# Optimization experiments

Hardware: AMD Instinct MI355X
Metric: run time of the kernel (lower is better)

## Reference

```python
import jax, jax.numpy as jnp
import numpy as np

RADIUS = 0.1
WEIGHT = 0.2
MATMUL_NORM = False


def setup_inputs() -> dict:
    key = jax.random.key(0)
    k1, k2, k3, k4, k5 = jax.random.split(key, 5)
    S, B, Ck, Cv, H, W = 8, 2, 64, 64, 64, 64
    return {
        "memory_keys": jax.random.normal(k1, (S, B, Ck, H, W), jnp.float32),
        "memory_values": jax.random.normal(k2, (S, B, Cv, H, W), jnp.float32),
        "query_query": jax.random.normal(k3, (B, Ck, H, W), jnp.float32),
        "disparity": jax.random.normal(k4, (B, 1, H, W), jnp.float32),
        "sequence_index": jax.random.randint(k5, (B, S, 2), 0, 10, jnp.int32),
    }


def reference(memory_keys, memory_values, query_query, disparity, sequence_index):
    S, B, Ck, H, W = memory_keys.shape
    Cv = memory_values.shape[2]
    HW, SHW = H * W, S * H * W

    # keys: [B, Ck, S*H*W]; queries: [B, H*W, Ck]
    keys = jnp.transpose(memory_keys, (1, 2, 0, 3, 4)).reshape(B, Ck, SHW)
    q = jnp.transpose(query_query.reshape(B, Ck, HW), (0, 2, 1))

    # disparity-based additive mask, vectorized over frames
    weight = WEIGHT / S / H / W
    idx = sequence_index.astype(jnp.float32)
    dist = jnp.sqrt((idx[:, :, 1] - 5.0) ** 2 + (idx[:, :, 0] - 5.0) ** 2)  # [B, S]
    total_disp = dist[:, :, None, None] * disparity  # [B, S, H, W] (disparity [B,1,H,W])
    mask = jnp.where(jnp.abs(total_disp) > RADIUS, weight, 0.0).reshape(B, 1, SHW)

    attn = jnp.einsum("bnc,bcm->bnm", q, keys)  # [B, HW, SHW]
    if MATMUL_NORM:
        attn = attn * (Ck ** -0.5)
    attn = jax.nn.softmax(attn, axis=-1) + mask

    vals = jnp.transpose(memory_values, (1, 0, 3, 4, 2)).reshape(B, SHW, Cv)
    out = jnp.einsum("bnm,bmv->bnv", attn, vals)  # [B, HW, Cv]
    return jnp.transpose(out, (0, 2, 1)).reshape(B, Cv, H, W)
```

## Files before the change

### kernel.cpp

```cpp
#include <hip/hip_runtime.h>
#include <hip/hip_bf16.h>
#include <stdint.h>

#define NS   8
#define NB   2
#define CK   64
#define CV   64
#define HWN  4096
#define SHW  32768
#define RADIUS_ 0.1f
#define MASK_W  6.103515625e-6f

#define TM    32
#define NW    8
#define QS_STR 68
#define P_STR  40
#define SBIAS 24.0f
#define LOG2E 1.4426950408889634f
#define SBIAS2 34.624680981135326f
#define KS    4

#define KT_ELEMS (NS * NB * CK * HWN)
#define KT_BYTES ((size_t)KT_ELEMS * 2)
#define VB_BYTES ((size_t)KT_ELEMS * 2)
#define MASK_OFF (KT_BYTES + VB_BYTES)
#define WS_NEED  (MASK_OFF + (size_t)NB * CV * 4)
#define ONUM_OFF (MASK_OFF + 4096)
#define ONUM_BYTES ((size_t)KS * NB * HWN * CV * 4)
#define ODEN_OFF (ONUM_OFF + ONUM_BYTES)
#define ODEN_BYTES ((size_t)KS * NB * HWN * 4)
#define WS2      (ODEN_OFF + ODEN_BYTES)

typedef __bf16    bf16x8 __attribute__((ext_vector_type(8)));
typedef _Float16  f16x8  __attribute__((ext_vector_type(8)));
typedef float     f32x4  __attribute__((ext_vector_type(4)));
typedef unsigned short u16x8 __attribute__((ext_vector_type(8)));
typedef uint32_t  u32x2 __attribute__((ext_vector_type(2)));
typedef uint32_t  u32x4 __attribute__((ext_vector_type(4)));

__device__ __forceinline__ unsigned short f2bfu(float x) {
  __hip_bfloat16 h = __float2bfloat16(x);
  return __builtin_bit_cast(unsigned short, h);
}
__device__ __forceinline__ bf16x8 ld_bf8_lds(const unsigned short* p) {
  u16x8 u = *(const u16x8*)p;
  return __builtin_bit_cast(bf16x8, u);
}
__device__ __forceinline__ void load_lds16(const void* g, void* l) {
  __builtin_amdgcn_global_load_lds(
      (const __attribute__((address_space(1))) unsigned int*)g,
      (__attribute__((address_space(3))) unsigned int*)l, 16, 0, 0);
}

#define PK_STR 72
__global__ __launch_bounds__(512) void prep_all(
    const float* __restrict__ keys, const float* __restrict__ vals,
    const float* __restrict__ disp, const int* __restrict__ seq,
    _Float16* __restrict__ kT, unsigned short* __restrict__ vbf,
    float* __restrict__ maskadd)
{
  const int t = threadIdx.x;
  const int blk = blockIdx.x;
  if (blk < 256) {
    __shared__ _Float16 lds[256 * PK_STR];
    const int chunk = blk & 15;
    const int s     = (blk >> 4) & 7;
    const int b     = blk >> 7;
    const int hw0   = chunk * 256;
    const int c_st  = t >> 3;
    const int msub  = (t & 7) * 8;

    const float* krow = keys + ((size_t)((s * NB + b) * CK + c_st)) * HWN + hw0;
    #pragma unroll
    for (int r = 0; r < 4; ++r) {
      const int m0 = msub + r * 64;
      f32x4 k0 = *(const f32x4*)(krow + m0);
      f32x4 k1 = *(const f32x4*)(krow + m0 + 4);
      #pragma unroll
      for (int j = 0; j < 4; ++j) {
        lds[(m0 + j)     * PK_STR + c_st] = (_Float16)k0[j];
        lds[(m0 + 4 + j) * PK_STR + c_st] = (_Float16)k1[j];
      }
    }
    __syncthreads();

    _Float16* kout = kT + ((size_t)(b * SHW + s * HWN + hw0)) * CK;
    const int mm = t >> 3, c0 = (t & 7) * 8;
    #pragma unroll
    for (int r2 = 0; r2 < 4; ++r2) {
      const int m = mm + r2 * 64;
      u16x8 v = *(const u16x8*)&lds[m * PK_STR + c0];
      *(u16x8*)(kout + (size_t)m * CK + c0) = v;
    }
  } else {
    const int r = blk - 256;
    const int s = r >> 7;
    const int b = (r >> 6) & 1;
    const int c = r & 63;
    float j0 = (float)seq[(b * NS + s) * 2 + 0];
    float j1 = (float)seq[(b * NS + s) * 2 + 1];
    const float dist = sqrtf((j1 - 5.f) * (j1 - 5.f) + (j0 - 5.f) * (j0 - 5.f));

    const size_t i = (size_t)r * HWN + t * 8;
    const int hw = t * 8;
    f32x4 a  = *(const f32x4*)(vals + i);
    f32x4 bb = *(const f32x4*)(vals + i + 4);
    f32x4 d0 = *(const f32x4*)(disp + (size_t)b * HWN + hw);
    f32x4 d1 = *(const f32x4*)(disp + (size_t)b * HWN + hw + 4);
    u16x8 o;
    float acc = 0.f;
    #pragma unroll
    for (int j = 0; j < 4; ++j) {
      o[j]     = f2bfu(a[j]);
      o[4 + j] = f2bfu(bb[j]);
      if (fabsf(dist * d0[j]) > RADIUS_) acc += a[j];
      if (fabsf(dist * d1[j]) > RADIUS_) acc += bb[j];
    }
    *(u16x8*)(vbf + i) = o;

    #pragma unroll
    for (int m = 32; m >= 1; m >>= 1) acc += __shfl_xor(acc, m);
    __shared__ float red[8];
    if ((t & 63) == 0) red[t >> 6] = acc;
    __syncthreads();
    if (t == 0) {
      float s8 = 0.f;
      #pragma unroll
      for (int j = 0; j < 8; ++j) s8 += red[j];
      atomicAdd(&maskadd[b * CV + c], MASK_W * s8);
    }
  }
}

struct __align__(16) Smem6 {
  union {
    struct {
      _Float16       kbuf[2][128 * 64];
      unsigned short vbuf[2][64 * 128];
    } main;
    struct {
      float obuf[4][32][64];
      float dbuf[4][32];
    } epi;
    float qs[64 * QS_STR];
  };
};

__global__ __launch_bounds__(512, 4) void attn_v6(
    const _Float16* __restrict__ kT,
    const unsigned short* __restrict__ vbf,
    const float* __restrict__ query,
    float* __restrict__ onum,
    float* __restrict__ odenom)
{
  __shared__ Smem6 sm;
  const int t    = threadIdx.x;
  const int w    = t >> 6;
  const int lane = t & 63;
  const int quad = lane >> 4;
  const int l15  = lane & 15;
  const int kq   = w & 3;
  const int rg   = w >> 2;
  const int bidx = blockIdx.x;
  const int xcd  = bidx & 7;
  const int b    = xcd & 1;
  const int ks   = xcd >> 1;
  const int tile = bidx >> 3;
  const int n0   = tile * 64;

  {
    const int qc   = t >> 3;
    const int noff = (t & 7) * 8;
    const int slot = qc ^ ((t & 7) << 2);
    const float* qp = query + (size_t)(b * CK + qc) * HWN + n0 + noff;
    f32x4 q0 = *(const f32x4*)(qp);
    f32x4 q1 = *(const f32x4*)(qp + 4);
    #pragma unroll
    for (int j = 0; j < 4; ++j) {
      sm.qs[(noff + j)     * QS_STR + slot] = q0[j];
      sm.qs[(noff + 4 + j) * QS_STR + slot] = q1[j];
    }
  }
  __syncthreads();
  f16x8 qf[2][2];
  #pragma unroll
  for (int f = 0; f < 2; ++f) {
    const int n  = rg * 32 + f * 16 + l15;
    const int sw = ((n >> 3) & 7) << 2;
    const float* base = &sm.qs[n * QS_STR];
    #pragma unroll
    for (int h = 0; h < 2; ++h) {
      const int c0 = (h * 32 + quad * 8) ^ sw;
      f32x4 a  = *(const f32x4*)(base + c0);
      f32x4 bb = *(const f32x4*)(base + (c0 ^ 4));
      f16x8 q;
      #pragma unroll
      for (int j = 0; j < 4; ++j) {
        q[j]     = (_Float16)(a[j]  * LOG2E);
        q[4 + j] = (_Float16)(bb[j] * LOG2E);
      }
      qf[f][h] = q;
    }
  }
  __syncthreads();

  f32x4 Of[2][4];
  f32x4 Ol[2];
  #pragma unroll
  for (int f = 0; f < 2; ++f) {
    #pragma unroll
    for (int cf = 0; cf < 4; ++cf) Of[f][cf] = (f32x4){0.f, 0.f, 0.f, 0.f};
    Ol[f] = (f32x4){0.f, 0.f, 0.f, 0.f};
  }
  bf16x8 vones;
  #pragma unroll
  for (int i = 0; i < 8; ++i)
    vones[i] = __builtin_bit_cast(__bf16, (unsigned short)0x3F80);

  uint32_t ksrc_off[2];
  int      kldsoff[2];
  uint32_t vsrc_off[2];
  int      vldsoff[2];
  #pragma unroll
  for (int j = 0; j < 2; ++j) {
    const int inst = w * 2 + j;
    const int kl   = inst * 8 + (lane >> 3);
    const int cqs  = lane & 7;
    ksrc_off[j] = (uint32_t)(kl * 128 + ((cqs ^ (kl & 7)) * 16));
    kldsoff[j]  = inst * 1024;
    const int cv  = inst * 4 + (lane >> 4);
    const int chs = (lane & 15) ^ (cv & 7);
    vsrc_off[j] = (uint32_t)(cv * HWN + chs * 8);
    vldsoff[j]  = inst * 1024;
  }
  const char* kgbase = (const char*)(kT + (size_t)b * SHW * CK);
  const int   kbase0 = ks * (SHW / KS);

  {
    const char* kg = kgbase + (size_t)kbase0 * 128;
    load_lds16(kg + ksrc_off[0], (char*)sm.main.kbuf[0] + kldsoff[0]);
    load_lds16(kg + ksrc_off[1], (char*)sm.main.kbuf[0] + kldsoff[1]);
    const int sfrm0 = kbase0 >> 12;
    const unsigned short* vg =
        vbf + (size_t)((sfrm0 * NB + b) * CV) * HWN + (kbase0 & 4095);
    load_lds16(vg + vsrc_off[0], (char*)sm.main.vbuf[0] + vldsoff[0]);
    load_lds16(vg + vsrc_off[1], (char*)sm.main.vbuf[0] + vldsoff[1]);
  }

  for (int it = 0; it < 64; ++it) {
    const int cur  = it & 1;
    const int key0 = kbase0 + it * 128;

    __syncthreads();

    if (it < 63) {
      const int keyn = key0 + 128;
      const char* kg = kgbase + (size_t)keyn * 128;
      load_lds16(kg + ksrc_off[0], (char*)sm.main.kbuf[cur ^ 1] + kldsoff[0]);
      load_lds16(kg + ksrc_off[1], (char*)sm.main.kbuf[cur ^ 1] + kldsoff[1]);
      const int sfrmn = keyn >> 12;
      const unsigned short* vg =
          vbf + (size_t)((sfrmn * NB + b) * CV) * HWN + (keyn & 4095);
      load_lds16(vg + vsrc_off[0], (char*)sm.main.vbuf[cur ^ 1] + vldsoff[0]);
      load_lds16(vg + vsrc_off[1], (char*)sm.main.vbuf[cur ^ 1] + vldsoff[1]);
    }

    f16x8 kf[2][2];
    #pragma unroll
    for (int g = 0; g < 2; ++g) {
      const int kl  = kq * 32 + g * 16 + l15;
      const int swz = kl & 7;
      const _Float16* kb = &sm.main.kbuf[cur][kl * 64];
      #pragma unroll
      for (int h = 0; h < 2; ++h) {
        const int slot = (h * 4 + quad) ^ swz;
        kf[g][h] = *(const f16x8*)(kb + slot * 8);
      }
    }

    bf16x8 vf[4];
    {
      const int c0 = kq * 4 + (quad >> 1);
      const int ho = (quad & 1) * 4;
      #pragma unroll
      for (int cf = 0; cf < 4; ++cf) {
        const int cv  = cf * 16 + l15;
        const int swz = cv & 7;
        const unsigned short* row = &sm.main.vbuf[cur][cv * 128];
        u32x2 lo = *(const u32x2*)(row + ((c0       ^ swz) * 8) + ho);
        u32x2 hi = *(const u32x2*)(row + (((c0 + 2) ^ swz) * 8) + ho);
        vf[cf] = __builtin_bit_cast(bf16x8, (u32x4){lo.x, lo.y, hi.x, hi.y});
      }
    }

    f32x4 sf[2][2];
    #pragma unroll
    for (int g = 0; g < 2; ++g)
      #pragma unroll
      for (int f = 0; f < 2; ++f) {
        f32x4 acc = (f32x4){-SBIAS2, -SBIAS2, -SBIAS2, -SBIAS2};
        acc = __builtin_amdgcn_mfma_f32_16x16x32_f16(kf[g][0], qf[f][0], acc, 0, 0, 0);
        acc = __builtin_amdgcn_mfma_f32_16x16x32_f16(kf[g][1], qf[f][1], acc, 0, 0, 0);
        sf[g][f] = acc;
      }

    #pragma unroll
    for (int f = 0; f < 2; ++f) {
      uint32_t pk[2][2];
      #pragma unroll
      for (int g = 0; g < 2; ++g) {
        float e0 = __builtin_amdgcn_exp2f(sf[g][f][0]);
        float e1 = __builtin_amdgcn_exp2f(sf[g][f][1]);
        float e2 = __builtin_amdgcn_exp2f(sf[g][f][2]);
        float e3 = __builtin_amdgcn_exp2f(sf[g][f][3]);
        pk[g][0] = __builtin_amdgcn_perm(__builtin_bit_cast(uint32_t, e1),
                                         __builtin_bit_cast(uint32_t, e0),
                                         0x07060302u);
        pk[g][1] = __builtin_amdgcn_perm(__builtin_bit_cast(uint32_t, e3),
                                         __builtin_bit_cast(uint32_t, e2),
                                         0x07060302u);
      }
      bf16x8 pf = __builtin_bit_cast(bf16x8,
          (u32x4){pk[0][0], pk[0][1], pk[1][0], pk[1][1]});

      #pragma unroll
      for (int cf = 0; cf < 4; ++cf)
        Of[f][cf] = __builtin_amdgcn_mfma_f32_16x16x32_bf16(pf, vf[cf], Of[f][cf], 0, 0, 0);
      Ol[f] = __builtin_amdgcn_mfma_f32_16x16x32_bf16(pf, vones, Ol[f], 0, 0, 0);
    }
  }

  __syncthreads();

  #pragma unroll
  for (int phase = 0; phase < 2; ++phase) {
    if (rg == phase) {
      #pragma unroll
      for (int f = 0; f < 2; ++f)
        #pragma unroll
        for (int r = 0; r < 4; ++r) {
          const int row = f * 16 + quad * 4 + r;
          if (l15 == 0) sm.epi.dbuf[kq][row] = Ol[f][r];
          #pragma unroll
          for (int cf = 0; cf < 4; ++cf)
            sm.epi.obuf[kq][row][cf * 16 + l15] = Of[f][cf][r];
        }
    }
    __syncthreads();
    {
      const int row = t >> 4;
      const int v4  = (t & 15) * 4;
      f32x4 acc = *(const f32x4*)&sm.epi.obuf[0][row][v4];
      #pragma unroll
      for (int q = 1; q < 4; ++q)
        acc += *(const f32x4*)&sm.epi.obuf[q][row][v4];
      *(f32x4*)&onum[((size_t)(ks * NB + b) * HWN + n0 + phase * 32 + row) * CV + v4] = acc;
      if (t < 32) {
        float d = sm.epi.dbuf[0][t] + sm.epi.dbuf[1][t] +
                  sm.epi.dbuf[2][t] + sm.epi.dbuf[3][t];
        odenom[(size_t)(ks * NB + b) * HWN + n0 + phase * 32 + t] = d;
      }
    }
    __syncthreads();
  }
}

__global__ __launch_bounds__(256) void finalize_k(
    const float* __restrict__ onum, const float* __restrict__ odenom,
    const float* __restrict__ maskadd, float* __restrict__ out)
{
  __shared__ float tile[64][68];
  __shared__ float dinv[64];
  __shared__ float ml[64];
  const int t   = threadIdx.x;
  const int b   = blockIdx.x >> 6;
  const int hw0 = (blockIdx.x & 63) * 64;

  #pragma unroll
  for (int pass = 0; pass < 4; ++pass) {
    const int row = pass * 16 + (t >> 4);
    const int v4  = (t & 15) * 4;
    f32x4 acc = (f32x4){0.f, 0.f, 0.f, 0.f};
    #pragma unroll
    for (int ks = 0; ks < KS; ++ks)
      acc += *(const f32x4*)&onum[((size_t)(ks * NB + b) * HWN + hw0 + row) * CV + v4];
    *(f32x4*)&tile[row][v4] = acc;
  }
  if (t < 64) {
    float d = 0.f;
    #pragma unroll
    for (int ks = 0; ks < KS; ++ks)
      d += odenom[(size_t)(ks * NB + b) * HWN + hw0 + t];
    dinv[t] = 1.f / fmaxf(d, 1e-30f);
  }
  if (t >= 64 && t < 128) ml[t - 64] = maskadd[b * CV + (t - 64)];
  __syncthreads();

  #pragma unroll
  for (int pass = 0; pass < 4; ++pass) {
    const int v   = pass * 16 + (t >> 4);
    const int hw4 = (t & 15) * 4;
    f32x4 o;
    #pragma unroll
    for (int j = 0; j < 4; ++j)
      o[j] = tile[hw4 + j][v] * dinv[hw4 + j] + ml[v];
    *(f32x4*)&out[((size_t)(b * CV + v)) * HWN + hw0 + hw4] = o;
  }
}

struct __align__(16) SmemF {
  union {
    float qs[TM * QS_STR];
    unsigned short p[NW][2][16 * P_STR];
    struct {
      float obuf[NW][TM][CV];
      float lbuf[NW][TM];
    } epi;
  };
};

__global__ __launch_bounds__(512) void attn_fast(
    const _Float16* __restrict__ kT, const unsigned short* __restrict__ vbf,
    const float* __restrict__ query, const float* __restrict__ maskadd,
    float* __restrict__ out)
{
  __shared__ SmemF sm;
  const int t    = threadIdx.x;
  const int w    = t >> 6;
  const int lane = t & 63;
  const int quad = lane >> 4;
  const int l15  = lane & 15;
  const int bidx = blockIdx.x;
  const int b    = bidx & 1;
  const int n0   = ((bidx >> 1) & 127) * TM;

  if (t < 256) {
    const int qc   = t >> 2;
    const int noff = (t & 3) * 8;
    const int slot = qc ^ ((t & 3) << 2);
    const float* qp = query + (size_t)(b * CK + qc) * HWN + n0 + noff;
    f32x4 q0 = *(const f32x4*)(qp);
    f32x4 q1 = *(const f32x4*)(qp + 4);
    #pragma unroll
    for (int j = 0; j < 4; ++j) {
      sm.qs[(noff + j)     * QS_STR + slot] = q0[j];
      sm.qs[(noff + 4 + j) * QS_STR + slot] = q1[j];
    }
  }
  __syncthreads();
  f16x8 qf[2][2];
  #pragma unroll
  for (int f = 0; f < 2; ++f) {
    const int n  = f * 16 + l15;
    const int sw = ((n >> 3) & 7) << 2;
    const float* base = &sm.qs[n * QS_STR];
    #pragma unroll
    for (int h = 0; h < 2; ++h) {
      const int c0 = (h * 32 + quad * 8) ^ sw;
      f32x4 a  = *(const f32x4*)(base + c0);
      f32x4 bb = *(const f32x4*)(base + (c0 ^ 4));
      f16x8 q;
      #pragma unroll
      for (int j = 0; j < 4; ++j) { q[j] = (_Float16)a[j]; q[4 + j] = (_Float16)bb[j]; }
      qf[f][h] = q;
    }
  }
  __syncthreads();

  f32x4 Of[2][4];
  f32x4 Ol[2];
  #pragma unroll
  for (int f = 0; f < 2; ++f) {
    #pragma unroll
    for (int cf = 0; cf < 4; ++cf) Of[f][cf] = (f32x4){0.f, 0.f, 0.f, 0.f};
    Ol[f] = (f32x4){0.f, 0.f, 0.f, 0.f};
  }
  bf16x8 vones;
  #pragma unroll
  for (int i = 0; i < 8; ++i)
    vones[i] = __builtin_bit_cast(__bf16, (unsigned short)0x3F80);

  const _Float16* kbase = kT + (size_t)b * SHW * CK;

  for (int it = 0; it < SHW / 256; ++it) {
    const int key0 = it * 256 + w * 32;
    f16x8 kf[2][2];
    #pragma unroll
    for (int g = 0; g < 2; ++g)
      #pragma unroll
      for (int h = 0; h < 2; ++h)
        kf[g][h] = *(const f16x8*)(kbase +
            (size_t)(key0 + g * 16 + l15) * CK + h * 32 + quad * 8);

    const int s   = it >> 4;
    const int hwv = (it & 15) * 256 + w * 32 + quad * 8;
    bf16x8 vf[4];
    #pragma unroll
    for (int cf = 0; cf < 4; ++cf)
      vf[cf] = ld_bf8_lds(vbf +
          ((size_t)((s * NB + b) * CV + cf * 16 + l15)) * HWN + hwv);

    f32x4 sfv[2][2];
    #pragma unroll
    for (int f = 0; f < 2; ++f)
      #pragma unroll
      for (int g = 0; g < 2; ++g) {
        f32x4 acc = (f32x4){0.f, 0.f, 0.f, 0.f};
        acc = __builtin_amdgcn_mfma_f32_16x16x32_f16(qf[f][0], kf[g][0], acc, 0, 0, 0);
        acc = __builtin_amdgcn_mfma_f32_16x16x32_f16(qf[f][1], kf[g][1], acc, 0, 0, 0);
        sfv[f][g] = acc;
      }

    #pragma unroll
    for (int f = 0; f < 2; ++f)
      #pragma unroll
      for (int g = 0; g < 2; ++g)
        #pragma unroll
        for (int r = 0; r < 4; ++r)
          sfv[f][g][r] = __expf(sfv[f][g][r] - SBIAS);

    #pragma unroll
    for (int f = 0; f < 2; ++f)
      #pragma unroll
      for (int g = 0; g < 2; ++g)
        #pragma unroll
        for (int r = 0; r < 4; ++r)
          sm.p[w][f][(quad * 4 + r) * P_STR + g * 16 + l15] = f2bfu(sfv[f][g][r]);
    asm volatile("s_waitcnt lgkmcnt(0)" ::: "memory");
    bf16x8 pf[2];
    #pragma unroll
    for (int f = 0; f < 2; ++f)
      pf[f] = ld_bf8_lds(&sm.p[w][f][l15 * P_STR + quad * 8]);

    #pragma unroll
    for (int f = 0; f < 2; ++f) {
      #pragma unroll
      for (int cf = 0; cf < 4; ++cf)
        Of[f][cf] = __builtin_amdgcn_mfma_f32_16x16x32_bf16(pf[f], vf[cf], Of[f][cf], 0, 0, 0);
      Ol[f] = __builtin_amdgcn_mfma_f32_16x16x32_bf16(pf[f], vones, Ol[f], 0, 0, 0);
    }
  }

  __syncthreads();
  #pragma unroll
  for (int f = 0; f < 2; ++f)
    #pragma unroll
    for (int r = 0; r < 4; ++r) {
      const int row = f * 16 + quad * 4 + r;
      if (l15 == 0) sm.epi.lbuf[w][row] = Ol[f][r];
      #pragma unroll
      for (int cf = 0; cf < 4; ++cf)
        sm.epi.obuf[w][row][cf * 16 + l15] = Of[f][cf][r];
    }
  __syncthreads();
  {
    const int n   = t & 31;
    const int vhi = t >> 5;
    float denom = 0.f;
    #pragma unroll
    for (int ww = 0; ww < NW; ++ww) denom += sm.epi.lbuf[ww][n];
    const float inv = 1.f / fmaxf(denom, 1e-30f);
    #pragma unroll
    for (int g = 0; g < 4; ++g) {
      const int v = vhi + 16 * g;
      float num = 0.f;
      #pragma unroll
      for (int ww = 0; ww < NW; ++ww) num += sm.epi.obuf[ww][n][v];
      out[((size_t)(b * CV + v)) * HWN + n0 + n] = num * inv + maskadd[b * CV + v];
    }
  }
}

extern "C" void kernel_launch(void* const* d_in, const int* in_sizes, int n_in,
                              void* d_out, int out_size, void* d_ws, size_t ws_size,
                              hipStream_t stream) {
  const float* keys  = (const float*)d_in[0];
  const float* vals  = (const float*)d_in[1];
  const float* query = (const float*)d_in[2];
  const float* disp  = (const float*)d_in[3];
  const int*   seq   = (const int*)d_in[4];
  float*       out   = (float*)d_out;

  _Float16*       kT   = (_Float16*)d_ws;
  unsigned short* vbf  = (unsigned short*)((char*)d_ws + KT_BYTES);
  float*          mask = (float*)((char*)d_ws + MASK_OFF);

  hipMemsetAsync(mask, 0, (size_t)NB * CV * 4, stream);
  prep_all<<<256 + NB * NS * CV, 512, 0, stream>>>(keys, vals, disp, seq, kT, vbf, mask);

  if (ws_size >= WS2) {
    float* onum   = (float*)((char*)d_ws + ONUM_OFF);
    float* odenom = (float*)((char*)d_ws + ODEN_OFF);
    attn_v6<<<NB * 64 * KS, 512, 0, stream>>>(kT, vbf, query, onum, odenom);
    finalize_k<<<NB * (HWN / 64), 256, 0, stream>>>(onum, odenom, mask, out);
  } else {
    attn_fast<<<NB * (HWN / TM), 512, 0, stream>>>(kT, vbf, query, mask, out);
  }
}
```

Before: 172.3 us.

## Load key fragments directly from global into registers, bypassing LDS

```diff
diff --git a/kernel.cpp b/kernel.cpp
--- a/kernel.cpp
+++ b/kernel.cpp
@@ -135,7 +135,6 @@
 struct __align__(16) Smem6 {
   union {
     struct {
-      _Float16       kbuf[2][128 * 64];
       unsigned short vbuf[2][64 * 128];
     } main;
     struct {
@@ -145,6 +144,58 @@
     float qs[64 * QS_STR];
   };
 };
+
+#define COMPUTE_TILE(CUR, KF)                                                  \
+  {                                                                            \
+    bf16x8 vf[4];                                                              \
+    {                                                                          \
+      const int c0 = kq * 4 + (quad >> 1);                                     \
+      const int ho = (quad & 1) * 4;                                           \
+      _Pragma("unroll")                                                        \
+      for (int cf = 0; cf < 4; ++cf) {                                         \
+        const int cv  = cf * 16 + l15;                                         \
+        const int swz = cv & 7;                                                \
+        const unsigned short* row = &sm.main.vbuf[CUR][cv * 128];              \
+        u32x2 lo = *(const u32x2*)(row + ((c0       ^ swz) * 8) + ho);         \
+        u32x2 hi = *(const u32x2*)(row + (((c0 + 2) ^ swz) * 8) + ho);         \
+        vf[cf] = __builtin_bit_cast(bf16x8, (u32x4){lo.x, lo.y, hi.x, hi.y});  \
+      }                                                                        \
+    }                                                                          \
+    f32x4 sf[2][2];                                                            \
+    _Pragma("unroll")                                                          \
+    for (int g = 0; g < 2; ++g) {                                              \
+      _Pragma("unroll")                                                        \
+      for (int f = 0; f < 2; ++f) {                                            \
+        f32x4 acc = (f32x4){-SBIAS2, -SBIAS2, -SBIAS2, -SBIAS2};               \
+        acc = __builtin_amdgcn_mfma_f32_16x16x32_f16(KF[g][0], qf[f][0], acc, 0, 0, 0); \
+        acc = __builtin_amdgcn_mfma_f32_16x16x32_f16(KF[g][1], qf[f][1], acc, 0, 0, 0); \
+        sf[g][f] = acc;                                                        \
+      }                                                                        \
+    }                                                                          \
+    _Pragma("unroll")                                                          \
+    for (int f = 0; f < 2; ++f) {                                              \
+      uint32_t pk[2][2];                                                       \
+      _Pragma("unroll")                                                        \
+      for (int g = 0; g < 2; ++g) {                                            \
+        float e0 = __builtin_amdgcn_exp2f(sf[g][f][0]);                        \
+        float e1 = __builtin_amdgcn_exp2f(sf[g][f][1]);                        \
+        float e2 = __builtin_amdgcn_exp2f(sf[g][f][2]);                        \
+        float e3 = __builtin_amdgcn_exp2f(sf[g][f][3]);                        \
+        pk[g][0] = __builtin_amdgcn_perm(__builtin_bit_cast(uint32_t, e1),     \
+                                         __builtin_bit_cast(uint32_t, e0),     \
+                                         0x07060302u);                         \
+        pk[g][1] = __builtin_amdgcn_perm(__builtin_bit_cast(uint32_t, e3),     \
+                                         __builtin_bit_cast(uint32_t, e2),     \
+                                         0x07060302u);                         \
+      }                                                                        \
+      bf16x8 pf = __builtin_bit_cast(bf16x8,                                   \
+          (u32x4){pk[0][0], pk[0][1], pk[1][0], pk[1][1]});                    \
+      _Pragma("unroll")                                                        \
+      for (int cf = 0; cf < 4; ++cf)                                           \
+        Of[f][cf] = __builtin_amdgcn_mfma_f32_16x16x32_bf16(pf, vf[cf], Of[f][cf], 0, 0, 0); \
+      Ol[f] = __builtin_amdgcn_mfma_f32_16x16x32_bf16(pf, vones, Ol[f], 0, 0, 0); \
+    }                                                                          \
+  }
 
 __global__ __launch_bounds__(512, 4) void attn_v6(
     const _Float16* __restrict__ kT,
@@ -217,29 +268,29 @@
   for (int i = 0; i < 8; ++i)
     vones[i] = __builtin_bit_cast(__bf16, (unsigned short)0x3F80);
 
-  uint32_t ksrc_off[2];
-  int      kldsoff[2];
   uint32_t vsrc_off[2];
   int      vldsoff[2];
   #pragma unroll
   for (int j = 0; j < 2; ++j) {
     const int inst = w * 2 + j;
-    const int kl   = inst * 8 + (lane >> 3);
-    const int cqs  = lane & 7;
-    ksrc_off[j] = (uint32_t)(kl * 128 + ((cqs ^ (kl & 7)) * 16));
-    kldsoff[j]  = inst * 1024;
     const int cv  = inst * 4 + (lane >> 4);
     const int chs = (lane & 15) ^ (cv & 7);
     vsrc_off[j] = (uint32_t)(cv * HWN + chs * 8);
     vldsoff[j]  = inst * 1024;
   }
-  const char* kgbase = (const char*)(kT + (size_t)b * SHW * CK);
-  const int   kbase0 = ks * (SHW / KS);
+  const int kbase0 = ks * (SHW / KS);
+
+  const _Float16* kg = kT + (size_t)b * SHW * CK
+                     + (size_t)(kbase0 + kq * 32 + l15) * CK + quad * 8;
+  f16x8 kfA[2][2], kfB[2][2];
+  #pragma unroll
+  for (int g = 0; g < 2; ++g)
+    #pragma unroll
+    for (int h = 0; h < 2; ++h)
+      kfA[g][h] = *(const f16x8*)(kg + g * (16 * CK) + h * 32);
+  const _Float16* kgn = kg + 128 * CK;
 
   {
-    const char* kg = kgbase + (size_t)kbase0 * 128;
-    load_lds16(kg + ksrc_off[0], (char*)sm.main.kbuf[0] + kldsoff[0]);
-    load_lds16(kg + ksrc_off[1], (char*)sm.main.kbuf[0] + kldsoff[1]);
     const int sfrm0 = kbase0 >> 12;
     const unsigned short* vg =
         vbf + (size_t)((sfrm0 * NB + b) * CV) * HWN + (kbase0 & 4095);
@@ -247,87 +298,44 @@
     load_lds16(vg + vsrc_off[1], (char*)sm.main.vbuf[0] + vldsoff[1]);
   }
 
-  for (int it = 0; it < 64; ++it) {
-    const int cur  = it & 1;
-    const int key0 = kbase0 + it * 128;
+  for (int itp = 0; itp < 32; ++itp) {
+    const int it0 = itp * 2;
 
     __syncthreads();
-
-    if (it < 63) {
-      const int keyn = key0 + 128;
-      const char* kg = kgbase + (size_t)keyn * 128;
-      load_lds16(kg + ksrc_off[0], (char*)sm.main.kbuf[cur ^ 1] + kldsoff[0]);
-      load_lds16(kg + ksrc_off[1], (char*)sm.main.kbuf[cur ^ 1] + kldsoff[1]);
+    {
+      const int keyn  = kbase0 + (it0 + 1) * 128;
       const int sfrmn = keyn >> 12;
       const unsigned short* vg =
           vbf + (size_t)((sfrmn * NB + b) * CV) * HWN + (keyn & 4095);
-      load_lds16(vg + vsrc_off[0], (char*)sm.main.vbuf[cur ^ 1] + vldsoff[0]);
-      load_lds16(vg + vsrc_off[1], (char*)sm.main.vbuf[cur ^ 1] + vldsoff[1]);
-    }
-
-    f16x8 kf[2][2];
-    #pragma unroll
-    for (int g = 0; g < 2; ++g) {
-      const int kl  = kq * 32 + g * 16 + l15;
-      const int swz = kl & 7;
-      const _Float16* kb = &sm.main.kbuf[cur][kl * 64];
-      #pragma unroll
-      for (int h = 0; h < 2; ++h) {
-        const int slot = (h * 4 + quad) ^ swz;
-        kf[g][h] = *(const f16x8*)(kb + slot * 8);
-      }
-    }
-
-    bf16x8 vf[4];
-    {
-      const int c0 = kq * 4 + (quad >> 1);
-      const int ho = (quad & 1) * 4;
-      #pragma unroll
-      for (int cf = 0; cf < 4; ++cf) {
-        const int cv  = cf * 16 + l15;
-        const int swz = cv & 7;
-        const unsigned short* row = &sm.main.vbuf[cur][cv * 128];
-        u32x2 lo = *(const u32x2*)(row + ((c0       ^ swz) * 8) + ho);
-        u32x2 hi = *(const u32x2*)(row + (((c0 + 2) ^ swz) * 8) + ho);
-        vf[cf] = __builtin_bit_cast(bf16x8, (u32x4){lo.x, lo.y, hi.x, hi.y});
-      }
-    }
-
-    f32x4 sf[2][2];
+      load_lds16(vg + vsrc_off[0], (char*)sm.main.vbuf[1] + vldsoff[0]);
+      load_lds16(vg + vsrc_off[1], (char*)sm.main.vbuf[1] + vldsoff[1]);
+    }
     #pragma unroll
     for (int g = 0; g < 2; ++g)
       #pragma unroll
-      for (int f = 0; f < 2; ++f) {
-        f32x4 acc = (f32x4){-SBIAS2, -SBIAS2, -SBIAS2, -SBIAS2};
-        acc = __builtin_amdgcn_mfma_f32_16x16x32_f16(kf[g][0], qf[f][0], acc, 0, 0, 0);
-        acc = __builtin_amdgcn_mfma_f32_16x16x32_f16(kf[g][1], qf[f][1], acc, 0, 0, 0);
-        sf[g][f] = acc;
-      }
-
-    #pragma unroll
-    for (int f = 0; f < 2; ++f) {
-      uint32_t pk[2][2];
-      #pragma unroll
-      for (int g = 0; g < 2; ++g) {
-        float e0 = __builtin_amdgcn_exp2f(sf[g][f][0]);
-        float e1 = __builtin_amdgcn_exp2f(sf[g][f][1]);
-        float e2 = __builtin_amdgcn_exp2f(sf[g][f][2]);
-        float e3 = __builtin_amdgcn_exp2f(sf[g][f][3]);
-        pk[g][0] = __builtin_amdgcn_perm(__builtin_bit_cast(uint32_t, e1),
-                                         __builtin_bit_cast(uint32_t, e0),
-                                         0x07060302u);
-        pk[g][1] = __builtin_amdgcn_perm(__builtin_bit_cast(uint32_t, e3),
-                                         __builtin_bit_cast(uint32_t, e2),
-                                         0x07060302u);
-      }
-      bf16x8 pf = __builtin_bit_cast(bf16x8,
-          (u32x4){pk[0][0], pk[0][1], pk[1][0], pk[1][1]});
-
-      #pragma unroll
-      for (int cf = 0; cf < 4; ++cf)
-        Of[f][cf] = __builtin_amdgcn_mfma_f32_16x16x32_bf16(pf, vf[cf], Of[f][cf], 0, 0, 0);
-      Ol[f] = __builtin_amdgcn_mfma_f32_16x16x32_bf16(pf, vones, Ol[f], 0, 0, 0);
-    }
+      for (int h = 0; h < 2; ++h)
+        kfB[g][h] = *(const f16x8*)(kgn + g * (16 * CK) + h * 32);
+    kgn += 128 * CK;
+
+    COMPUTE_TILE(0, kfA)
+
+    __syncthreads();
+    if (itp < 31) {
+      const int keyn  = kbase0 + (it0 + 2) * 128;
+      const int sfrmn = keyn >> 12;
+      const unsigned short* vg =
+          vbf + (size_t)((sfrmn * NB + b) * CV) * HWN + (keyn & 4095);
+      load_lds16(vg + vsrc_off[0], (char*)sm.main.vbuf[0] + vldsoff[0]);
+      load_lds16(vg + vsrc_off[1], (char*)sm.main.vbuf[0] + vldsoff[1]);
+      #pragma unroll
+      for (int g = 0; g < 2; ++g)
+        #pragma unroll
+        for (int h = 0; h < 2; ++h)
+          kfA[g][h] = *(const f16x8*)(kgn + g * (16 * CK) + h * 32);
+      kgn += 128 * CK;
+    }
+
+    COMPUTE_TILE(1, kfB)
   }
 
   __syncthreads();
```

New measurement: 234.6 us. 1.36x slower.

## Prefetch two tiles ahead with explicit vmcnt waits instead of full syncthreads drain

Applied to the files above, without the earlier changes.

```diff
diff --git a/kernel.cpp b/kernel.cpp
--- a/kernel.cpp
+++ b/kernel.cpp
@@ -236,34 +236,26 @@
   const char* kgbase = (const char*)(kT + (size_t)b * SHW * CK);
   const int   kbase0 = ks * (SHW / KS);
 
-  {
-    const char* kg = kgbase + (size_t)kbase0 * 128;
-    load_lds16(kg + ksrc_off[0], (char*)sm.main.kbuf[0] + kldsoff[0]);
-    load_lds16(kg + ksrc_off[1], (char*)sm.main.kbuf[0] + kldsoff[1]);
-    const int sfrm0 = kbase0 >> 12;
+  #pragma unroll
+  for (int pt = 0; pt < 2; ++pt) {
+    const int key0 = kbase0 + pt * 128;
+    const char* kg = kgbase + (size_t)key0 * 128;
+    load_lds16(kg + ksrc_off[0], (char*)sm.main.kbuf[pt] + kldsoff[0]);
+    load_lds16(kg + ksrc_off[1], (char*)sm.main.kbuf[pt] + kldsoff[1]);
+    const int sfrm = key0 >> 12;
     const unsigned short* vg =
-        vbf + (size_t)((sfrm0 * NB + b) * CV) * HWN + (kbase0 & 4095);
-    load_lds16(vg + vsrc_off[0], (char*)sm.main.vbuf[0] + vldsoff[0]);
-    load_lds16(vg + vsrc_off[1], (char*)sm.main.vbuf[0] + vldsoff[1]);
+        vbf + (size_t)((sfrm * NB + b) * CV) * HWN + (key0 & 4095);
+    load_lds16(vg + vsrc_off[0], (char*)sm.main.vbuf[pt] + vldsoff[0]);
+    load_lds16(vg + vsrc_off[1], (char*)sm.main.vbuf[pt] + vldsoff[1]);
   }
 
   for (int it = 0; it < 64; ++it) {
-    const int cur  = it & 1;
-    const int key0 = kbase0 + it * 128;
-
-    __syncthreads();
-
-    if (it < 63) {
-      const int keyn = key0 + 128;
-      const char* kg = kgbase + (size_t)keyn * 128;
-      load_lds16(kg + ksrc_off[0], (char*)sm.main.kbuf[cur ^ 1] + kldsoff[0]);
-      load_lds16(kg + ksrc_off[1], (char*)sm.main.kbuf[cur ^ 1] + kldsoff[1]);
-      const int sfrmn = keyn >> 12;
-      const unsigned short* vg =
-          vbf + (size_t)((sfrmn * NB + b) * CV) * HWN + (keyn & 4095);
-      load_lds16(vg + vsrc_off[0], (char*)sm.main.vbuf[cur ^ 1] + vldsoff[0]);
-      load_lds16(vg + vsrc_off[1], (char*)sm.main.vbuf[cur ^ 1] + vldsoff[1]);
-    }
+    const int cur = it & 1;
+
+    if (it < 63) asm volatile("s_waitcnt vmcnt(4)" ::: "memory");
+    else         asm volatile("s_waitcnt vmcnt(0)" ::: "memory");
+    __builtin_amdgcn_s_barrier();
+    __builtin_amdgcn_sched_barrier(0);
 
     f16x8 kf[2][2];
     #pragma unroll
@@ -327,6 +319,22 @@
       for (int cf = 0; cf < 4; ++cf)
         Of[f][cf] = __builtin_amdgcn_mfma_f32_16x16x32_bf16(pf, vf[cf], Of[f][cf], 0, 0, 0);
       Ol[f] = __builtin_amdgcn_mfma_f32_16x16x32_bf16(pf, vones, Ol[f], 0, 0, 0);
+    }
+
+    __builtin_amdgcn_sched_barrier(0);
+    __builtin_amdgcn_s_barrier();
+    __builtin_amdgcn_sched_barrier(0);
+
+    if (it < 62) {
+      const int keyn = kbase0 + (it + 2) * 128;
+      const char* kg = kgbase + (size_t)keyn * 128;
+      load_lds16(kg + ksrc_off[0], (char*)sm.main.kbuf[cur] + kldsoff[0]);
+      load_lds16(kg + ksrc_off[1], (char*)sm.main.kbuf[cur] + kldsoff[1]);
+      const int sfrmn = keyn >> 12;
+      const unsigned short* vg =
+          vbf + (size_t)((sfrmn * NB + b) * CV) * HWN + (keyn & 4095);
+      load_lds16(vg + vsrc_off[0], (char*)sm.main.vbuf[cur] + vldsoff[0]);
+      load_lds16(vg + vsrc_off[1], (char*)sm.main.vbuf[cur] + vldsoff[1]);
     }
   }
 
```

After: 174.5 us. No clear change (+1.3%).

## Fuse split-K finalize into attention kernel via last-block counter; drop mask memset

Applied to the files above, without the earlier changes.

```diff
diff --git a/kernel.cpp b/kernel.cpp
--- a/kernel.cpp
+++ b/kernel.cpp
@@ -23,9 +23,10 @@
 #define KT_ELEMS (NS * NB * CK * HWN)
 #define KT_BYTES ((size_t)KT_ELEMS * 2)
 #define VB_BYTES ((size_t)KT_ELEMS * 2)
-#define MASK_OFF (KT_BYTES + VB_BYTES)
-#define WS_NEED  (MASK_OFF + (size_t)NB * CV * 4)
-#define ONUM_OFF (MASK_OFF + 4096)
+#define MASKP_OFF (KT_BYTES + VB_BYTES)
+#define CNT_OFF  (MASKP_OFF + 4096)
+#define WS_NEED  (CNT_OFF + 4096)
+#define ONUM_OFF (CNT_OFF + 4096)
 #define ONUM_BYTES ((size_t)KS * NB * HWN * CV * 4)
 #define ODEN_OFF (ONUM_OFF + ONUM_BYTES)
 #define ODEN_BYTES ((size_t)KS * NB * HWN * 4)
@@ -57,11 +58,12 @@
     const float* __restrict__ keys, const float* __restrict__ vals,
     const float* __restrict__ disp, const int* __restrict__ seq,
     _Float16* __restrict__ kT, unsigned short* __restrict__ vbf,
-    float* __restrict__ maskadd)
+    float* __restrict__ maskpart, unsigned int* __restrict__ cnt)
 {
   const int t = threadIdx.x;
   const int blk = blockIdx.x;
   if (blk < 256) {
+    if (blk == 0 && t < NB * 64) cnt[t] = 0;
     __shared__ _Float16 lds[256 * PK_STR];
     const int chunk = blk & 15;
     const int s     = (blk >> 4) & 7;
@@ -127,7 +129,7 @@
       float s8 = 0.f;
       #pragma unroll
       for (int j = 0; j < 8; ++j) s8 += red[j];
-      atomicAdd(&maskadd[b * CV + c], MASK_W * s8);
+      maskpart[(b * CV + c) * NS + s] = MASK_W * s8;
     }
   }
 }
@@ -142,6 +144,11 @@
       float obuf[4][32][64];
       float dbuf[4][32];
     } epi;
+    struct {
+      float tile[64][68];
+      float dinv[64];
+      float ml[64];
+    } fin;
     float qs[64 * QS_STR];
   };
 };
@@ -151,9 +158,13 @@
     const unsigned short* __restrict__ vbf,
     const float* __restrict__ query,
     float* __restrict__ onum,
-    float* __restrict__ odenom)
+    float* __restrict__ odenom,
+    const float* __restrict__ maskpart,
+    unsigned int* __restrict__ cnt,
+    float* __restrict__ out)
 {
   __shared__ Smem6 sm;
+  __shared__ int lastflag;
   const int t    = threadIdx.x;
   const int w    = t >> 6;
   const int lane = t & 63;
@@ -363,48 +374,54 @@
     }
     __syncthreads();
   }
-}
-
-__global__ __launch_bounds__(256) void finalize_k(
-    const float* __restrict__ onum, const float* __restrict__ odenom,
-    const float* __restrict__ maskadd, float* __restrict__ out)
-{
-  __shared__ float tile[64][68];
-  __shared__ float dinv[64];
-  __shared__ float ml[64];
-  const int t   = threadIdx.x;
-  const int b   = blockIdx.x >> 6;
-  const int hw0 = (blockIdx.x & 63) * 64;
-
-  #pragma unroll
-  for (int pass = 0; pass < 4; ++pass) {
-    const int row = pass * 16 + (t >> 4);
-    const int v4  = (t & 15) * 4;
-    f32x4 acc = (f32x4){0.f, 0.f, 0.f, 0.f};
-    #pragma unroll
-    for (int ks = 0; ks < KS; ++ks)
-      acc += *(const f32x4*)&onum[((size_t)(ks * NB + b) * HWN + hw0 + row) * CV + v4];
-    *(f32x4*)&tile[row][v4] = acc;
-  }
-  if (t < 64) {
-    float d = 0.f;
-    #pragma unroll
-    for (int ks = 0; ks < KS; ++ks)
-      d += odenom[(size_t)(ks * NB + b) * HWN + hw0 + t];
-    dinv[t] = 1.f / fmaxf(d, 1e-30f);
-  }
-  if (t >= 64 && t < 128) ml[t - 64] = maskadd[b * CV + (t - 64)];
-  __syncthreads();
-
-  #pragma unroll
-  for (int pass = 0; pass < 4; ++pass) {
-    const int v   = pass * 16 + (t >> 4);
+
+  __threadfence();
+  if (t == 0) {
+    unsigned int old = atomicAdd(&cnt[b * 64 + tile], 1u);
+    lastflag = (old == KS - 1);
+  }
+  __syncthreads();
+  if (!lastflag) return;
+  __threadfence();
+
+  {
+    const int row = t >> 3;
+    const int c8  = (t & 7) * 8;
+    f32x4 a0 = (f32x4){0.f, 0.f, 0.f, 0.f};
+    f32x4 a1 = (f32x4){0.f, 0.f, 0.f, 0.f};
+    #pragma unroll
+    for (int q = 0; q < KS; ++q) {
+      const float* p = &onum[((size_t)(q * NB + b) * HWN + n0 + row) * CV + c8];
+      a0 += *(const f32x4*)(p);
+      a1 += *(const f32x4*)(p + 4);
+    }
+    *(f32x4*)&sm.fin.tile[row][c8]     = a0;
+    *(f32x4*)&sm.fin.tile[row][c8 + 4] = a1;
+    if ((t & 7) == 0) {
+      float d = 0.f;
+      #pragma unroll
+      for (int q = 0; q < KS; ++q)
+        d += odenom[(size_t)(q * NB + b) * HWN + n0 + row];
+      sm.fin.dinv[row] = 1.f / fmaxf(d, 1e-30f);
+    }
+    if (t < 64) {
+      float m = 0.f;
+      #pragma unroll
+      for (int s = 0; s < NS; ++s) m += maskpart[(b * CV + t) * NS + s];
+      sm.fin.ml[t] = m;
+    }
+  }
+  __syncthreads();
+
+  #pragma unroll
+  for (int pass = 0; pass < 2; ++pass) {
+    const int c   = pass * 32 + (t >> 4);
     const int hw4 = (t & 15) * 4;
     f32x4 o;
     #pragma unroll
     for (int j = 0; j < 4; ++j)
-      o[j] = tile[hw4 + j][v] * dinv[hw4 + j] + ml[v];
-    *(f32x4*)&out[((size_t)(b * CV + v)) * HWN + hw0 + hw4] = o;
+      o[j] = sm.fin.tile[hw4 + j][c] * sm.fin.dinv[hw4 + j] + sm.fin.ml[c];
+    *(f32x4*)&out[((size_t)(b * CV + c)) * HWN + n0 + hw4] = o;
   }
 }
 
@@ -421,7 +438,7 @@
 
 __global__ __launch_bounds__(512) void attn_fast(
     const _Float16* __restrict__ kT, const unsigned short* __restrict__ vbf,
-    const float* __restrict__ query, const float* __restrict__ maskadd,
+    const float* __restrict__ query, const float* __restrict__ maskpart,
     float* __restrict__ out)
 {
   __shared__ SmemF sm;
@@ -566,7 +583,10 @@
       float num = 0.f;
       #pragma unroll
       for (int ww = 0; ww < NW; ++ww) num += sm.epi.obuf[ww][n][v];
-      out[((size_t)(b * CV + v)) * HWN + n0 + n] = num * inv + maskadd[b * CV + v];
+      float ml = 0.f;
+      #pragma unroll
+      for (int s = 0; s < NS; ++s) ml += maskpart[(b * CV + v) * NS + s];
+      out[((size_t)(b * CV + v)) * HWN + n0 + n] = num * inv + ml;
     }
   }
 }
@@ -581,19 +601,20 @@
   const int*   seq   = (const int*)d_in[4];
   float*       out   = (float*)d_out;
 
-  _Float16*       kT   = (_Float16*)d_ws;
-  unsigned short* vbf  = (unsigned short*)((char*)d_ws + KT_BYTES);
-  float*          mask = (float*)((char*)d_ws + MASK_OFF);
-
-  hipMemsetAsync(mask, 0, (size_t)NB * CV * 4, stream);
-  prep_all<<<256 + NB * NS * CV, 512, 0, stream>>>(keys, vals, disp, seq, kT, vbf, mask);
+  _Float16*       kT    = (_Float16*)d_ws;
+  unsigned short* vbf   = (unsigned short*)((char*)d_ws + KT_BYTES);
+  float*          maskp = (float*)((char*)d_ws + MASKP_OFF);
+  unsigned int*   cnt   = (unsigned int*)((char*)d_ws + CNT_OFF);
+
+  prep_all<<<256 + NB * NS * CV, 512, 0, stream>>>(keys, vals, disp, seq,
+                                                   kT, vbf, maskp, cnt);
 
   if (ws_size >= WS2) {
     float* onum   = (float*)((char*)d_ws + ONUM_OFF);
     float* odenom = (float*)((char*)d_ws + ODEN_OFF);
-    attn_v6<<<NB * 64 * KS, 512, 0, stream>>>(kT, vbf, query, onum, odenom);
-    finalize_k<<<NB * (HWN / 64), 256, 0, stream>>>(onum, odenom, mask, out);
+    attn_v6<<<NB * 64 * KS, 512, 0, stream>>>(kT, vbf, query, onum, odenom,
+                                              maskp, cnt, out);
   } else {
-    attn_fast<<<NB * (HWN / TM), 512, 0, stream>>>(kT, vbf, query, mask, out);
+    attn_fast<<<NB * (HWN / TM), 512, 0, stream>>>(kT, vbf, query, maskp, out);
   }
 }
```

After: 295.9 us. 71.8% more time.
